# Performance work log

Measured on AMD Instinct MI355X. Metric: run time of the kernel, lower is better.

Reference implementation:

```python
import jax, jax.numpy as jnp
import numpy as np

N, C = 131072, 128
NUM_PREDICTORS = 8


def setup_inputs() -> dict:
    key = jax.random.key(0)
    ks = jax.random.split(key, 9)
    d = {f"outputs{i+1}": jax.random.normal(ks[i], (N, C), dtype=jnp.float32) for i in range(7)}
    d["mimic"] = jax.random.normal(ks[7], (N, C), dtype=jnp.float32)
    d["targets"] = jax.random.randint(ks[8], (N,), 0, C, dtype=jnp.int32)
    d["n_test"] = N
    return d


def _margin(x, targets):
    # x: [N, C]; top-2 margin if the target logit is the max, else 0 (ties by value equality, as in torch code)
    top2, _ = jax.lax.top_k(x, 2)                                  # [N, 2]
    tval = jnp.take_along_axis(x, targets[:, None], axis=1)[:, 0]  # [N]
    return jnp.where(tval == top2[:, 0], top2[:, 0] - top2[:, 1], jnp.zeros((), x.dtype))


def reference(outputs1, outputs2, outputs3, outputs4, outputs5, outputs6, outputs7, mimic, targets, n_test):
    T = 2.0
    preds = [outputs1, outputs2, outputs3, outputs4, outputs5, outputs6, outputs7, mimic]
    # [N, 8] margins, one column per predictor
    margins = jnp.stack([_margin(p, targets) for p in preds], axis=1)
    out_threshold = jax.nn.softmax(margins / T, axis=1)            # softmax over the 8 predictors per sample
    max_preds = jnp.max(jnp.stack(preds[:7], axis=0))              # global max over outputs1..7
    return max_preds, out_threshold
```

## Files before the change

### kernel.cpp

```cpp
#include <hip/hip_runtime.h>
#include <cfloat>

constexpr int kN = 131072;
constexpr int kC = 128;
constexpr int kRowsPerBlock = 64;

__device__ __forceinline__ unsigned fmap(float f) {
    unsigned b = __float_as_uint(f);
    return (b & 0x80000000u) ? ~b : (b | 0x80000000u);
}

template<int CTRL>
__device__ __forceinline__ float dppmov(float x) {
    return __int_as_float(__builtin_amdgcn_update_dpp(
        __float_as_int(x), __float_as_int(x), CTRL, 0xF, 0xF, false));
}

__device__ __forceinline__ void top2_merge(float& m1, float& m2, float o1, float o2) {
    const float lo = fminf(m1, o1);
    m1 = fmaxf(m1, o1);
    m2 = fmaxf(fmaxf(m2, o2), lo);
}

__global__ __launch_bounds__(256, 8) void margins_kernel(
    const float* __restrict__ p0, const float* __restrict__ p1,
    const float* __restrict__ p2, const float* __restrict__ p3,
    const float* __restrict__ p4, const float* __restrict__ p5,
    const float* __restrict__ p6, const float* __restrict__ p7,
    const int* __restrict__ targets, float* __restrict__ out,
    unsigned* __restrict__ gmax_ws)
{
    __shared__ float marg_lds[kRowsPerBlock][9];
    __shared__ unsigned blockmax;

    const int t = threadIdx.x;
    if (t == 0) blockmax = 0u;
    __syncthreads();

    const float* preds[8] = {p0, p1, p2, p3, p4, p5, p6, p7};

    const int l   = t & 63;
    const int w   = t >> 6;
    const int myl = l & 15;
    const int rg  = l >> 4;
    const int R0  = blockIdx.x * kRowsPerBlock + w * 16;

    const size_t base_off = ((size_t)(R0 + rg) * kC + myl * 4) * sizeof(float);

    int tg[4];
#pragma unroll
    for (int it = 0; it < 4; ++it) tg[it] = targets[R0 + it * 4 + rg];

    float gm = -FLT_MAX;

    float4 A[4], B[4];
#pragma unroll
    for (int g = 0; g < 4; ++g) {
        const char* p = (const char*)preds[g >> 2] + base_off
                      + (size_t)(g & 3) * 4 * kC * sizeof(float);
        A[g] = *(const float4*)p;
        B[g] = *(const float4*)(p + 256);
    }

#pragma unroll
    for (int g = 0; g < 32; ++g) {
        const int j  = g >> 2;
        const int it = g & 3;

        const float4 va = A[g & 3];
        const float4 vb = B[g & 3];

        if (g + 4 < 32) {
            const int gn = g + 4;
            const char* p = (const char*)preds[gn >> 2] + base_off
                          + (size_t)(gn & 3) * 4 * kC * sizeof(float);
            A[g & 3] = *(const float4*)p;
            B[g & 3] = *(const float4*)(p + 256);
        }
        __builtin_amdgcn_sched_barrier(0);

        float a1 = fmaxf(va.x, va.y), a2 = fminf(va.x, va.y);
        float b1 = fmaxf(va.z, va.w), b2 = fminf(va.z, va.w);
        const float mA1 = fmaxf(a1, b1);
        const float mA2 = fmaxf(fminf(a1, b1), fmaxf(a2, b2));
        a1 = fmaxf(vb.x, vb.y); a2 = fminf(vb.x, vb.y);
        b1 = fmaxf(vb.z, vb.w); b2 = fminf(vb.z, vb.w);
        const float mB1 = fmaxf(a1, b1);
        const float mB2 = fmaxf(fminf(a1, b1), fmaxf(a2, b2));
        float m1 = mA1, m2 = mA2;
        top2_merge(m1, m2, mB1, mB2);

        { const float o1 = dppmov<0xB1>(m1),  o2 = dppmov<0xB1>(m2);  top2_merge(m1, m2, o1, o2); }
        { const float o1 = dppmov<0x4E>(m1),  o2 = dppmov<0x4E>(m2);  top2_merge(m1, m2, o1, o2); }
        { const float o1 = dppmov<0x124>(m1), o2 = dppmov<0x124>(m2); top2_merge(m1, m2, o1, o2); }
        { const float o1 = dppmov<0x128>(m1), o2 = dppmov<0x128>(m2); top2_merge(m1, m2, o1, o2); }

        const int tt = tg[it];
        const float4 hv = (tt & 64) ? vb : va;
        const int el = tt & 3;
        const float tv = (el == 0) ? hv.x : (el == 1) ? hv.y : (el == 2) ? hv.z : hv.w;
        const float margin = (tv == m1) ? (m1 - m2) : 0.0f;
        if (myl == ((tt >> 2) & 15)) marg_lds[w * 16 + it * 4 + rg][j] = margin;
        if (j < 7) gm = fmaxf(gm, m1);
    }

    {
        const int rr = l >> 2;
        const int q  = l & 3;
        float m[8];
#pragma unroll
        for (int jj = 0; jj < 8; ++jj) m[jj] = marg_lds[w * 16 + rr][jj];
        float mm = m[0];
#pragma unroll
        for (int jj = 1; jj < 8; ++jj) mm = fmaxf(mm, m[jj]);
        float e[8], s = 0.0f;
#pragma unroll
        for (int jj = 0; jj < 8; ++jj) { e[jj] = __expf((m[jj] - mm) * 0.5f); s += e[jj]; }
        const float inv = 1.0f / s;
        const float o0 = ((q == 0) ? e[0] : (q == 1) ? e[2] : (q == 2) ? e[4] : e[6]) * inv;
        const float o1 = ((q == 0) ? e[1] : (q == 1) ? e[3] : (q == 2) ? e[5] : e[7]) * inv;
        const size_t ob = 1 + ((size_t)(blockIdx.x * kRowsPerBlock + w * 16 + rr)) * 8 + q * 2;
        out[ob]     = o0;
        out[ob + 1] = o1;
    }

    gm = fmaxf(gm, __shfl_xor(gm, 16));
    gm = fmaxf(gm, __shfl_xor(gm, 32));
    if (l == 0) atomicMax(&blockmax, fmap(gm));
    __syncthreads();
    if (t == 0) atomicMax(gmax_ws, blockmax);
}

__global__ void finalize_kernel(const unsigned* __restrict__ gmax_ws,
                                float* __restrict__ out)
{
    unsigned u = *gmax_ws;
    unsigned b = (u & 0x80000000u) ? (u & 0x7FFFFFFFu) : ~u;
    out[0] = __uint_as_float(b);
}

extern "C" void kernel_launch(void* const* d_in, const int* in_sizes, int n_in,
                              void* d_out, int out_size, void* d_ws, size_t ws_size,
                              hipStream_t stream) {
    const float* p0 = (const float*)d_in[0];
    const float* p1 = (const float*)d_in[1];
    const float* p2 = (const float*)d_in[2];
    const float* p3 = (const float*)d_in[3];
    const float* p4 = (const float*)d_in[4];
    const float* p5 = (const float*)d_in[5];
    const float* p6 = (const float*)d_in[6];
    const float* p7 = (const float*)d_in[7];
    const int* targets = (const int*)d_in[8];
    float* out = (float*)d_out;
    unsigned* ws = (unsigned*)d_ws;

    hipMemsetAsync(ws, 0, sizeof(unsigned), stream);

    dim3 grid(kN / kRowsPerBlock), block(256);
    margins_kernel<<<grid, block, 0, stream>>>(p0, p1, p2, p3, p4, p5, p6, p7,
                                               targets, out, ws);
    finalize_kernel<<<1, 1, 0, stream>>>(ws, out);
}
```

Baseline: 463.9 us.

## Use nontemporal double-buffered loads and fuse finalize into last-block atomic

Switches the input loads to nontemporal loads and cuts the software prefetch from four row-groups ahead to one (double buffering). The separate finalize kernel is removed: each block increments a counter after its atomicMax, and the last block converts and writes the global maximum. This lowers register pressure and saves one kernel launch. In exchange, fewer loads are in flight per wave, so less memory latency is hidden.

```diff
diff --git a/kernel.cpp b/kernel.cpp
--- a/kernel.cpp
+++ b/kernel.cpp
@@ -4,6 +4,9 @@
 constexpr int kN = 131072;
 constexpr int kC = 128;
 constexpr int kRowsPerBlock = 64;
+constexpr int kGrid = kN / kRowsPerBlock;
+
+typedef float vf4 __attribute__((ext_vector_type(4)));
 
 __device__ __forceinline__ unsigned fmap(float f) {
     unsigned b = __float_as_uint(f);
@@ -28,10 +31,11 @@
     const float* __restrict__ p4, const float* __restrict__ p5,
     const float* __restrict__ p6, const float* __restrict__ p7,
     const int* __restrict__ targets, float* __restrict__ out,
-    unsigned* __restrict__ gmax_ws)
+    unsigned* __restrict__ ws)
 {
     __shared__ float marg_lds[kRowsPerBlock][9];
     __shared__ unsigned blockmax;
+    __shared__ unsigned lastflag;
 
     const int t = threadIdx.x;
     if (t == 0) blockmax = 0u;
@@ -53,13 +57,11 @@
 
     float gm = -FLT_MAX;
 
-    float4 A[4], B[4];
-#pragma unroll
-    for (int g = 0; g < 4; ++g) {
-        const char* p = (const char*)preds[g >> 2] + base_off
-                      + (size_t)(g & 3) * 4 * kC * sizeof(float);
-        A[g] = *(const float4*)p;
-        B[g] = *(const float4*)(p + 256);
+    vf4 A[2], B[2];
+    {
+        const char* p = (const char*)preds[0] + base_off;
+        A[0] = __builtin_nontemporal_load((const vf4*)p);
+        B[0] = __builtin_nontemporal_load((const vf4*)(p + 256));
     }
 
 #pragma unroll
@@ -67,17 +69,18 @@
         const int j  = g >> 2;
         const int it = g & 3;
 
-        const float4 va = A[g & 3];
-        const float4 vb = B[g & 3];
-
-        if (g + 4 < 32) {
-            const int gn = g + 4;
-            const char* p = (const char*)preds[gn >> 2] + base_off
-                          + (size_t)(gn & 3) * 4 * kC * sizeof(float);
-            A[g & 3] = *(const float4*)p;
-            B[g & 3] = *(const float4*)(p + 256);
+        if (g < 31) {
+            const int jn  = (g + 1) >> 2;
+            const int itn = (g + 1) & 3;
+            const char* p = (const char*)preds[jn] + base_off
+                          + (size_t)itn * 4 * kC * sizeof(float);
+            A[(g + 1) & 1] = __builtin_nontemporal_load((const vf4*)p);
+            B[(g + 1) & 1] = __builtin_nontemporal_load((const vf4*)(p + 256));
         }
         __builtin_amdgcn_sched_barrier(0);
+
+        const vf4 va = A[g & 1];
+        const vf4 vb = B[g & 1];
 
         float a1 = fmaxf(va.x, va.y), a2 = fminf(va.x, va.y);
         float b1 = fmaxf(va.z, va.w), b2 = fminf(va.z, va.w);
@@ -96,7 +99,7 @@
         { const float o1 = dppmov<0x128>(m1), o2 = dppmov<0x128>(m2); top2_merge(m1, m2, o1, o2); }
 
         const int tt = tg[it];
-        const float4 hv = (tt & 64) ? vb : va;
+        const vf4 hv = (tt & 64) ? vb : va;
         const int el = tt & 3;
         const float tv = (el == 0) ? hv.x : (el == 1) ? hv.y : (el == 2) ? hv.z : hv.w;
         const float margin = (tv == m1) ? (m1 - m2) : 0.0f;
@@ -128,15 +131,19 @@
     gm = fmaxf(gm, __shfl_xor(gm, 32));
     if (l == 0) atomicMax(&blockmax, fmap(gm));
     __syncthreads();
-    if (t == 0) atomicMax(gmax_ws, blockmax);
-}
-
-__global__ void finalize_kernel(const unsigned* __restrict__ gmax_ws,
-                                float* __restrict__ out)
-{
-    unsigned u = *gmax_ws;
-    unsigned b = (u & 0x80000000u) ? (u & 0x7FFFFFFFu) : ~u;
-    out[0] = __uint_as_float(b);
+    if (t == 0) {
+        atomicMax(&ws[0], blockmax);
+        __threadfence();
+        const unsigned c = atomicAdd(&ws[1], 1u);
+        lastflag = (c == (unsigned)(kGrid - 1)) ? 1u : 0u;
+    }
+    __syncthreads();
+    if (t == 0 && lastflag) {
+        __threadfence();
+        const unsigned u = atomicMax(&ws[0], 0u);
+        const unsigned b = (u & 0x80000000u) ? (u & 0x7FFFFFFFu) : ~u;
+        out[0] = __uint_as_float(b);
+    }
 }
 
 extern "C" void kernel_launch(void* const* d_in, const int* in_sizes, int n_in,
@@ -154,10 +161,9 @@
     float* out = (float*)d_out;
     unsigned* ws = (unsigned*)d_ws;
 
-    hipMemsetAsync(ws, 0, sizeof(unsigned), stream);
+    hipMemsetAsync(ws, 0, 2 * sizeof(unsigned), stream);
 
-    dim3 grid(kN / kRowsPerBlock), block(256);
+    dim3 grid(kGrid), block(256);
     margins_kernel<<<grid, block, 0, stream>>>(p0, p1, p2, p3, p4, p5, p6, p7,
                                                targets, out, ws);
-    finalize_kernel<<<1, 1, 0, stream>>>(ws, out);
 }
```

New measurement: 504.4 us. 1.09x slower.
